# Optimization experiments

Hardware: AMD Instinct MI355X
Metric: run time of the kernel (lower is better)

The kernel has to match this reference:

```python
import jax, jax.numpy as jnp
import numpy as np

B, Q, K, D, H, HD, HID, ED, CPB, E = 2, 300, 1024, 256, 8, 32, 32, 256, 256, 131072
N = B * Q
EPS = 1e-5


def _ln(x, g, b):
    mu = x.mean(-1, keepdims=True)
    v = ((x - mu) ** 2).mean(-1, keepdims=True)
    return (x - mu) / jnp.sqrt(v + EPS) * g + b


def setup_inputs():
    key = jax.random.key(0)
    ks = jax.random.split(key, 32)
    rn = lambda k, s, sc=0.02: jax.random.normal(k, s, jnp.float32) * sc
    return {
        "nodes": jax.random.normal(ks[0], (N, D), jnp.float32),
        "images": jax.random.normal(ks[1], (B, K, D), jnp.float32),
        "rel_coords": jax.random.normal(ks[2], (B, Q, K, 2), jnp.float32),
        "edge_feats": jax.random.normal(ks[3], (E, ED), jnp.float32),
        "edge_index": jax.random.randint(ks[4], (2, E), 0, N, jnp.int32),
        "images_mask": jnp.zeros((B, K), dtype=bool),
        "ln1_g": jnp.ones((D,)), "ln1_b": jnp.zeros((D,)),
        "ln2_g": jnp.ones((D,)), "ln2_b": jnp.zeros((D,)),
        "ln3_g": jnp.ones((D,)), "ln3_b": jnp.zeros((D,)),
        "Wni": rn(ks[5], (D, HID * H)), "bni": jnp.zeros((HID * H,)),
        "Wnj": rn(ks[6], (D, HID * H)), "bnj": jnp.zeros((HID * H,)),
        "We": rn(ks[7], (ED, HID * H)), "be": jnp.zeros((HID * H,)),
        "attn_proj": jax.random.normal(ks[8], (H, HID), jnp.float32),
        "Wmsg": rn(ks[9], (D + ED, D)), "bmsg": jnp.zeros((D,)),
        "Wg_out": rn(ks[10], (D, D)), "bg_out": jnp.zeros((D,)),
        "Wq": rn(ks[11], (D, D)), "bq": jnp.zeros((D,)),
        "Wkv": rn(ks[12], (D, 2 * D)), "bkv": jnp.zeros((2 * D,)),
        "Wc1": rn(ks[13], (2, CPB), 0.5), "bc1": jnp.zeros((CPB,)),
        "Wc2": rn(ks[14], (CPB, H), 0.1), "bc2": jnp.zeros((H,)),
        "Wc_out": rn(ks[15], (D, D)), "bc_out": jnp.zeros((D,)),
        "Wf1": rn(ks[16], (D, 4 * D)), "bf1": jnp.zeros((4 * D,)),
        "Wf2": rn(ks[17], (4 * D, D)), "bf2": jnp.zeros((D,)),
    }


def reference(nodes, images, rel_coords, edge_feats, edge_index, images_mask,
              ln1_g, ln1_b, ln2_g, ln2_b, ln3_g, ln3_b,
              Wni, bni, Wnj, bnj, We, be, attn_proj, Wmsg, bmsg, Wg_out, bg_out,
              Wq, bq, Wkv, bkv, Wc1, bc1, Wc2, bc2, Wc_out, bc_out,
              Wf1, bf1, Wf2, bf2):
    src, dst = edge_index[0], edge_index[1]
    # --- graph attention (pre-LN residual) ---
    x = _ln(nodes, ln1_g, ln1_b)
    ni, nj = x[src], x[dst]  # [E, D]
    hidden = jax.nn.leaky_relu(
        ni @ Wni + bni + nj @ Wnj + bnj + edge_feats @ We + be, 0.2)
    hidden = hidden.reshape(E, H, HID)
    logits = jnp.einsum('ehd,hd->eh', hidden, attn_proj)  # [E, H]
    m = jax.ops.segment_max(logits, src, num_segments=N)
    z = jnp.exp(logits - m[src])
    scores = z / jax.ops.segment_sum(z, src, num_segments=N)[src]  # scatter softmax
    msg = (jnp.concatenate([nj, edge_feats], -1) @ Wmsg + bmsg).reshape(E, H, HD)
    agg = jax.ops.segment_sum(msg * scores[..., None], src, num_segments=N).reshape(N, D)
    nodes = nodes + (agg @ Wg_out + bg_out)
    # --- cross attention with continuous position bias ---
    x2 = _ln(nodes, ln2_g, ln2_b).reshape(B, Q, D)
    q = (x2 @ Wq + bq).reshape(B, Q, H, HD).transpose(0, 2, 1, 3)  # [B,H,Q,hd]
    kv = (images @ Wkv + bkv).reshape(B, K, 2, H, HD)
    k = kv[:, :, 0].transpose(0, 2, 1, 3)  # [B,H,K,hd]
    v = kv[:, :, 1].transpose(0, 2, 1, 3)
    cpb = jax.nn.relu(rel_coords @ Wc1 + bc1) @ Wc2 + bc2  # [B,Q,K,H]
    bias = jnp.where(images_mask[:, None, None, :], -jnp.inf,
                     jnp.transpose(cpb, (0, 3, 1, 2)))  # [B,H,Q,K]
    att = jnp.einsum('bhqd,bhkd->bhqk', q, k) / jnp.sqrt(jnp.float32(HD)) + bias
    p = jax.nn.softmax(att, axis=-1)
    out = jnp.einsum('bhqk,bhkd->bhqd', p, v)
    out = out.reshape(B, Q, H * HD)  # faithful to original: reshape WITHOUT head transpose
    nodes = nodes + (out @ Wc_out + bc_out).reshape(N, D)
    # --- FFN (residual from the normed input, as in original) ---
    x3 = _ln(nodes, ln3_g, ln3_b)
    ff = jax.nn.gelu(x3 @ Wf1 + bf1, approximate=False) @ Wf2 + bf2
    return ff + x3
```

## Files before the change

### kernel.cpp

```cpp
#include <hip/hip_runtime.h>
#include <hip/hip_bf16.h>
#include <math.h>

#define E_   131072
#define CH_  16384
#define N_   600
#define NB_  2
#define NQ_  300
#define NK_  1024
#define NH_  8

typedef __hip_bfloat16 bf16;
typedef __bf16 bh8 __attribute__((ext_vector_type(8)));
typedef float  fx4 __attribute__((ext_vector_type(4)));

static __device__ __forceinline__ float b2f(bf16 x){ return __bfloat162float(x); }
static __device__ __forceinline__ unsigned short bfu(float x){
  return __bfloat16_as_ushort(__float2bfloat16(x));
}
static __device__ __forceinline__ unsigned pack2(float x, float y){
  return (unsigned)bfu(x) | ((unsigned)bfu(y) << 16);
}
static __device__ __forceinline__ float ldf(const void* p, size_t i, bool isf32){
  return isf32 ? ((const float*)p)[i] : b2f(((const bf16*)p)[i]);
}

constexpr int WOFF[32] = {
  0,256,512,768,1024,1280,
  1536,67072,67328,132864,
  133120,133376,
  133632,264704,
  264960,330496,330752,396288,
  396544,527616,
  528128,528640,528896,530944,
  530952,596488,
  596744,858888,859912,1122056,
  1122312,
  1187848};
#define NWSEG 31
#define WTOT  1187848
struct SrcTab { const void* p[NWSEG]; };
struct TrTab { int4 d[8]; };

static __device__ __forceinline__ void ln_stats(float v, int t, float* r1, float* r2,
                                                float& mu, float& rstd){
  float s1 = v, s2 = v*v;
  #pragma unroll
  for (int o = 32; o; o >>= 1){ s1 += __shfl_down(s1, o); s2 += __shfl_down(s2, o); }
  if ((t & 63) == 0){ r1[t>>6] = s1; r2[t>>6] = s2; }
  __syncthreads();
  float t1 = r1[0]+r1[1]+r1[2]+r1[3];
  float t2 = r2[0]+r2[1]+r2[2]+r2[3];
  mu = t1 * (1.f/256.f);
  float var = t2 * (1.f/256.f) - mu*mu;
  rstd = rsqrtf(var + 1e-5f);
  __syncthreads();
}

__global__ void k_init(int* cnt, unsigned* mkey, float* denom,
                       const void* nodes, int* dflag){
  int i = blockIdx.x*256 + threadIdx.x;
  if (i < N_) cnt[i] = 0;
  if (i < N_*NH_){ mkey[i] = 0u; denom[i] = 0.f; }
  if (i == 0){
    const unsigned short* h = (const unsigned short*)nodes;
    int odd = 0;
    for (int j = 0; j < 64; j++){
      int e = (h[j] >> 7) & 0xFF;
      if (e < 100 || e > 150) odd++;
    }
    *dflag = (odd > 8) ? 1 : 0;
  }
}

__global__ __launch_bounds__(256) void k_cvt(SrcTab tab, float* wall, const int* dflag){
  int i = blockIdx.x*256 + threadIdx.x;
  if (i >= WTOT) return;
  bool isf32 = (*dflag != 0);
  int seg = 0;
  while (seg < NWSEG-1 && i >= WOFF[seg+1]) seg++;
  wall[i] = ldf(tab.p[seg], (size_t)(i - WOFF[seg]), isf32);
}

__global__ __launch_bounds__(256) void k_tr(TrTab tab, const float* __restrict__ wall,
                                            bf16* __restrict__ wbt)
{
  __shared__ float tile[64][65];
  int4 d = tab.d[blockIdx.z];
  int K = d.y, Nn = d.z;
  int k0 = blockIdx.x*64, n0 = blockIdx.y*64;
  if (k0 >= K || n0 >= Nn) return;
  const float* src = wall + d.x;
  bf16* dst = wbt + d.w;
  int t = threadIdx.x;
  int rr = t >> 6, cc = t & 63;
  #pragma unroll
  for (int p = 0; p < 16; p++){
    int row = p*4 + rr;
    tile[row][cc] = src[(size_t)(k0 + row)*Nn + n0 + cc];
  }
  __syncthreads();
  #pragma unroll
  for (int p = 0; p < 16; p++){
    int row = p*4 + rr;
    dst[(size_t)(n0 + row)*K + k0 + cc] = __float2bfloat16(tile[cc][row]);
  }
}

__global__ __launch_bounds__(256) void k_ln1(
    const void* __restrict__ nodes, const int* __restrict__ dflag,
    const float* __restrict__ g1, const float* __restrict__ b1, bf16* __restrict__ x1)
{
  __shared__ float r1[4], r2[4];
  int n = blockIdx.x, t = threadIdx.x;
  bool isf32 = (*dflag != 0);
  float v = ldf(nodes, (size_t)n*256 + t, isf32);
  float mu, rstd;
  ln_stats(v, t, r1, r2, mu, rstd);
  x1[n*256 + t] = __float2bfloat16((v - mu) * rstd * g1[t] + b1[t]);
}

__global__ void k_count(const int* __restrict__ ei, int* cnt){
  int e = blockIdx.x*256 + threadIdx.x;
  atomicAdd(&cnt[ei[e]], 1);
}

__global__ __launch_bounds__(1024) void k_scan(const int* __restrict__ cnt,
                                               int* offs, int* cursor){
  __shared__ int s[1024];
  int t = threadIdx.x;
  s[t] = (t < N_) ? cnt[t] : 0;
  __syncthreads();
  for (int o = 1; o < 1024; o <<= 1){
    int v = 0;
    if (t >= o) v = s[t - o];
    __syncthreads();
    if (t >= o) s[t] += v;
    __syncthreads();
  }
  if (t < N_){ int excl = (t == 0) ? 0 : s[t-1]; offs[t] = excl; cursor[t] = excl; }
  if (t == N_-1) offs[N_] = s[N_-1];
}

__global__ void k_scatter(const int* __restrict__ ei, int* cursor, int* eorder){
  int e = blockIdx.x*256 + threadIdx.x;
  int pos = atomicAdd(&cursor[ei[e]], 1);
  eorder[pos] = e;
}

__global__ __launch_bounds__(256) void k_gemm_dual(
    const void* __restrict__ A, int m_base, const int* __restrict__ dflag,
    const bf16* __restrict__ BT, bf16* __restrict__ C)
{
  __shared__ __align__(16) bf16 As[128*40];
  __shared__ __align__(16) bf16 Bs[128*40];
  int m0 = blockIdx.x * 128;
  int n0 = blockIdx.y * 128;
  int t = threadIdx.x;
  bool isf32 = (*dflag != 0);
  int wave = t >> 6, lane = t & 63;
  int wr = (wave >> 1) * 64, wc = (wave & 1) * 64;
  int lm = lane & 15, lq = lane >> 4;
  int srow = t >> 2;
  int scol = (t & 3) * 8;
  size_t r0 = (size_t)(m_base + m0 + srow) * 256;
  size_t r1 = (size_t)(m_base + m0 + 64 + srow) * 256;
  fx4 acc[4][4] = {};
  for (int kk = 0; kk < 256; kk += 32){
    uint4 pa0, pa1;
    if (isf32){
      const float* a0p = (const float*)A + r0 + kk + scol;
      const float* a1p = (const float*)A + r1 + kk + scol;
      float4 va0a = *(const float4*)(a0p);
      float4 va0b = *(const float4*)(a0p + 4);
      float4 va1a = *(const float4*)(a1p);
      float4 va1b = *(const float4*)(a1p + 4);
      pa0.x = pack2(va0a.x, va0a.y); pa0.y = pack2(va0a.z, va0a.w);
      pa0.z = pack2(va0b.x, va0b.y); pa0.w = pack2(va0b.z, va0b.w);
      pa1.x = pack2(va1a.x, va1a.y); pa1.y = pack2(va1a.z, va1a.w);
      pa1.z = pack2(va1b.x, va1b.y); pa1.w = pack2(va1b.z, va1b.w);
    } else {
      pa0 = *(const uint4*)((const bf16*)A + r0 + kk + scol);
      pa1 = *(const uint4*)((const bf16*)A + r1 + kk + scol);
    }
    float4 vb0 = *(const float4*)(BT + (size_t)(n0 + srow)      * 256 + kk + scol);
    float4 vb1 = *(const float4*)(BT + (size_t)(n0 + 64 + srow) * 256 + kk + scol);
    __syncthreads();
    *(uint4*)(As + srow*40 + scol)         = pa0;
    *(uint4*)(As + (64 + srow)*40 + scol)  = pa1;
    *(float4*)(Bs + srow*40 + scol)        = vb0;
    *(float4*)(Bs + (64 + srow)*40 + scol) = vb1;
    __syncthreads();
    bh8 af[4], bfr[4];
    #pragma unroll
    for (int mt = 0; mt < 4; mt++)
      af[mt] = *reinterpret_cast<const bh8*>(As + (wr + mt*16 + lm)*40 + lq*8);
    #pragma unroll
    for (int nt = 0; nt < 4; nt++)
      bfr[nt] = *reinterpret_cast<const bh8*>(Bs + (wc + nt*16 + lm)*40 + lq*8);
    #pragma unroll
    for (int mt = 0; mt < 4; mt++)
      #pragma unroll
      for (int nt = 0; nt < 4; nt++)
        acc[mt][nt] = __builtin_amdgcn_mfma_f32_16x16x32_bf16(af[mt], bfr[nt], acc[mt][nt], 0, 0, 0);
  }
  #pragma unroll
  for (int mt = 0; mt < 4; mt++)
    #pragma unroll
    for (int nt = 0; nt < 4; nt++)
      #pragma unroll
      for (int r = 0; r < 4; r++){
        int row = m0 + wr + mt*16 + lq*4 + r;
        int col = n0 + wc + nt*16 + lm;
        C[(size_t)row*256 + col] = __float2bfloat16(acc[mt][nt][r]);
      }
}

__global__ __launch_bounds__(256) void k_gemm(
    const void* __restrict__ A, const int* __restrict__ dflag, int adual,
    int K, int M, const bf16* __restrict__ BT, int mode,
    void* __restrict__ D, int ldd,
    const float* __restrict__ bias, const float* __restrict__ add,
    float* __restrict__ aux)
{
  __shared__ __align__(16) bf16 As[128*40];
  __shared__ __align__(16) bf16 Bs[128*40];
  int m0 = blockIdx.x * 128;
  int n0 = blockIdx.y * 128;
  int t = threadIdx.x;
  bool f32src = adual && (*dflag != 0);
  int wave = t >> 6, lane = t & 63;
  int wr = (wave >> 1) * 64, wc = (wave & 1) * 64;
  int lm = lane & 15, lq = lane >> 4;
  int srow = t >> 2;
  int scol = (t & 3) * 8;
  size_t rA0 = (size_t)(m0 + srow) * K;
  size_t rA1 = (size_t)(m0 + 64 + srow) * K;
  size_t rB0 = (size_t)(n0 + srow) * K;
  size_t rB1 = (size_t)(n0 + 64 + srow) * K;
  fx4 acc[4][4] = {};
  for (int kk = 0; kk < K; kk += 32){
    uint4 pa0, pa1;
    if (f32src){
      const float* a0p = (const float*)A + rA0 + kk + scol;
      const float* a1p = (const float*)A + rA1 + kk + scol;
      float4 a = *(const float4*)(a0p), b = *(const float4*)(a0p + 4);
      float4 c = *(const float4*)(a1p), d = *(const float4*)(a1p + 4);
      pa0.x = pack2(a.x,a.y); pa0.y = pack2(a.z,a.w);
      pa0.z = pack2(b.x,b.y); pa0.w = pack2(b.z,b.w);
      pa1.x = pack2(c.x,c.y); pa1.y = pack2(c.z,c.w);
      pa1.z = pack2(d.x,d.y); pa1.w = pack2(d.z,d.w);
    } else {
      pa0 = *(const uint4*)((const bf16*)A + rA0 + kk + scol);
      pa1 = *(const uint4*)((const bf16*)A + rA1 + kk + scol);
    }
    float4 vb0 = *(const float4*)(BT + rB0 + kk + scol);
    float4 vb1 = *(const float4*)(BT + rB1 + kk + scol);
    __syncthreads();
    *(uint4*)(As + srow*40 + scol)         = pa0;
    *(uint4*)(As + (64 + srow)*40 + scol)  = pa1;
    *(float4*)(Bs + srow*40 + scol)        = vb0;
    *(float4*)(Bs + (64 + srow)*40 + scol) = vb1;
    __syncthreads();
    bh8 af[4], bfr[4];
    #pragma unroll
    for (int mt = 0; mt < 4; mt++)
      af[mt] = *reinterpret_cast<const bh8*>(As + (wr + mt*16 + lm)*40 + lq*8);
    #pragma unroll
    for (int nt = 0; nt < 4; nt++)
      bfr[nt] = *reinterpret_cast<const bh8*>(Bs + (wc + nt*16 + lm)*40 + lq*8);
    #pragma unroll
    for (int mt = 0; mt < 4; mt++)
      #pragma unroll
      for (int nt = 0; nt < 4; nt++)
        acc[mt][nt] = __builtin_amdgcn_mfma_f32_16x16x32_bf16(af[mt], bfr[nt], acc[mt][nt], 0, 0, 0);
  }
  #pragma unroll
  for (int mt = 0; mt < 4; mt++)
    #pragma unroll
    for (int nt = 0; nt < 4; nt++)
      #pragma unroll
      for (int r = 0; r < 4; r++){
        int row = m0 + wr + mt*16 + lq*4 + r;
        int col = n0 + wc + nt*16 + lm;
        if (row >= M) continue;
        float v = acc[mt][nt][r];
        if (mode == 0){
          if (bias) v += bias[col];
          ((float*)D)[(size_t)row*ldd + col] = v;
        } else if (mode == 1){
          v += bias[col];
          if (col < 256){
            ((float*)D)[(size_t)row*256 + col] = v;
          } else {
            int b = row >> 10, ki = row & 1023;
            int hh = (col - 256) >> 5, dd = (col - 256) & 31;
            aux[(((size_t)b*NH_ + hh)*32 + dd)*NK_ + ki] = v;
          }
        } else if (mode == 2){
          v += bias[col] + add[(size_t)row*ldd + col];
          ((float*)D)[(size_t)row*ldd + col] = v;
        } else {
          v += bias[col];
          float g = 0.5f*v*(1.f + erff(v*0.70710678118654752f));
          ((bf16*)D)[(size_t)row*ldd + col] = __float2bfloat16(g);
        }
      }
}

__global__ __launch_bounds__(256) void k_logits(
    const bf16* __restrict__ He, const float* __restrict__ Pall,
    const float* __restrict__ bni, const float* __restrict__ bnj, const float* __restrict__ be,
    const float* __restrict__ ap, const int* __restrict__ ei,
    float* __restrict__ logits, unsigned* __restrict__ mkey, int e0chunk)
{
  __shared__ float hs[32*264];
  __shared__ int   ssh[32], dsh[32];
  __shared__ float aps[256], bhs[256];
  int t = threadIdx.x;
  int base = e0chunk + blockIdx.x*32;
  if (t < 32) ssh[t] = ei[base + t];
  else if (t < 64) dsh[t-32] = ei[E_ + base + (t - 32)];
  aps[t] = ap[t];
  bhs[t] = bni[t] + bnj[t] + be[t];
  __syncthreads();
  int slot = (t >> 5)*33 + (t & 31);
  for (int r = 0; r < 32; r++){
    float v = b2f(He[(size_t)(base - e0chunk + r)*256 + t])
            + Pall[ssh[r]*768 + t] + Pall[dsh[r]*768 + 256 + t] + bhs[t];
    v = (v > 0.f) ? v : 0.2f*v;
    hs[r*264 + slot] = v;
  }
  __syncthreads();
  int e = t >> 3, h = t & 7;
  const float* hr  = hs + e*264 + h*33;
  const float* apr = aps + h*32;
  float acc = 0.f;
  #pragma unroll
  for (int i = 0; i < 32; i++) acc = fmaf(hr[i], apr[i], acc);
  logits[(size_t)(base + e)*8 + h] = acc;
  unsigned ub = __float_as_uint(acc);
  unsigned key = (ub & 0x80000000u) ? ~ub : (ub | 0x80000000u);
  atomicMax(&mkey[ssh[e]*8 + h], key);
}

__global__ __launch_bounds__(256) void k_softden(
    const int* __restrict__ ei, float* __restrict__ logits,
    const unsigned* __restrict__ mkey, float* __restrict__ denom)
{
  int gid = blockIdx.x*256 + threadIdx.x;
  int e = gid >> 3, h = gid & 7;
  int s = ei[e];
  unsigned key = mkey[s*8 + h];
  unsigned ub = (key & 0x80000000u) ? (key & 0x7FFFFFFFu) : ~key;
  float m = __uint_as_float(ub);
  float a = fminf(logits[gid] - m, 0.f);
  float z = __expf(a);
  logits[gid] = z;
  atomicAdd(&denom[s*8 + h], z);
}

__global__ __launch_bounds__(256) void k_agg(
    const int* __restrict__ offs, const int* __restrict__ eorder, const int* __restrict__ ei,
    const float* __restrict__ z, const float* __restrict__ denom,
    const void* __restrict__ ef, const int* __restrict__ dflag,
    const float* __restrict__ Pall,
    const float* __restrict__ bmsg, const float* __restrict__ Wmsg,
    const void* __restrict__ nodes,
    const float* __restrict__ Wg, const float* __restrict__ bg,
    const float* __restrict__ g2, const float* __restrict__ b2v,
    const float* __restrict__ Wq, const float* __restrict__ bq,
    float* __restrict__ nodes1, float* __restrict__ qbuf)
{
  __shared__ __align__(16) bf16 efs[256*40];
  __shared__ __align__(16) bf16 za[16*40];
  __shared__ float zsh[32*8];
  __shared__ int   esh[32], dsh[32];
  __shared__ float Fs[8*257];
  __shared__ float aggs[256];
  __shared__ float sinv[8];
  __shared__ float r1[4], r2[4];
  int n = blockIdx.x, t = threadIdx.x;
  bool isf32 = (*dflag != 0);
  int wave = t >> 6, lane = t & 63;
  int lm = lane & 15, lq = lane >> 4;
  int h = t >> 5;
  int jz = t >> 3, hz = t & 7;
  int e0 = offs[n], e1 = offs[n+1];
  if (t < 8){
    float ds = denom[n*8 + t];
    sinv[t] = (ds > 0.f) ? 1.f/ds : 0.f;
  }
  fx4 acc[4] = {};
  float gacc = 0.f;
  for (int base = e0; base < e1; base += 32){
    int cnt = min(32, e1 - base);
    __syncthreads();
    if (t < 32){
      int e = (t < cnt) ? eorder[base + t] : eorder[e0];
      esh[t] = e; dsh[t] = ei[E_ + e];
    }
    __syncthreads();
    float zv = (jz < cnt) ? z[(size_t)esh[jz]*8 + hz] : 0.f;
    zsh[t] = zv;
    za[hz*40 + jz] = __float2bfloat16(zv);
    za[(8 + hz)*40 + jz] = (bf16)0.f;
    #pragma unroll
    for (int rb = 0; rb < 32; rb += 4){
      float v0 = ldf(ef, (size_t)esh[rb+0]*256 + t, isf32);
      float v1 = ldf(ef, (size_t)esh[rb+1]*256 + t, isf32);
      float v2 = ldf(ef, (size_t)esh[rb+2]*256 + t, isf32);
      float v3 = ldf(ef, (size_t)esh[rb+3]*256 + t, isf32);
      ushort4 pk = { bfu(v0), bfu(v1), bfu(v2), bfu(v3) };
      *(ushort4*)&efs[t*40 + rb] = pk;
    }
    __syncthreads();
    #pragma unroll 8
    for (int jj = 0; jj < 32; jj++)
      gacc = fmaf(zsh[jj*8 + h], Pall[(size_t)dsh[jj]*768 + 512 + t], gacc);
    bh8 afrag = *reinterpret_cast<const bh8*>(za + lm*40 + lq*8);
    #pragma unroll
    for (int tile = 0; tile < 4; tile++){
      int coln = wave*64 + tile*16 + lm;
      bh8 bfrag = *reinterpret_cast<const bh8*>(efs + coln*40 + lq*8);
      acc[tile] = __builtin_amdgcn_mfma_f32_16x16x32_bf16(afrag, bfrag, acc[tile], 0, 0, 0);
    }
  }
  __syncthreads();
  #pragma unroll
  for (int tile = 0; tile < 4; tile++)
    #pragma unroll
    for (int r = 0; r < 4; r++){
      int row = lq*4 + r;
      if (row < 8){
        int col = wave*64 + tile*16 + lm;
        Fs[row*257 + col] = acc[tile][r] * sinv[row];
      }
    }
  __syncthreads();
  float am = gacc * sinv[h] + bmsg[t];
  const float* fr = Fs + h*257;
  for (int k = 0; k < 256; k++)
    am = fmaf(fr[k], Wmsg[(size_t)(256 + k)*256 + t], am);
  aggs[t] = am;
  __syncthreads();
  float o = bg[t] + ldf(nodes, (size_t)n*256 + t, isf32);
  for (int k = 0; k < 256; k++) o = fmaf(aggs[k], Wg[k*256 + t], o);
  nodes1[n*256 + t] = o;
  float mu, rstd;
  ln_stats(o, t, r1, r2, mu, rstd);
  float x2 = (o - mu) * rstd * g2[t] + b2v[t];
  __syncthreads();
  aggs[t] = x2;
  __syncthreads();
  float q = bq[t];
  for (int k = 0; k < 256; k++) q = fmaf(aggs[k], Wq[k*256 + t], q);
  qbuf[n*256 + t] = q;
}

__global__ __launch_bounds__(256) void k_cpb(
    const void* __restrict__ rel, const int* __restrict__ dflag,
    const float* __restrict__ Wc1, const float* __restrict__ bc1,
    const float* __restrict__ Wc2, const float* __restrict__ bc2, bf16* __restrict__ bias)
{
  __shared__ float w0[256], w1[256], bb[256], w2[256*8], b2s[8];
  int t = threadIdx.x;
  bool isf32 = (*dflag != 0);
  w0[t] = Wc1[t]; w1[t] = Wc1[256 + t]; bb[t] = bc1[t];
  for (int i = t; i < 2048; i += 256) w2[i] = Wc2[i];
  if (t < 8) b2s[t] = bc2[t];
  __syncthreads();
  size_t pos = (size_t)blockIdx.x*256 + t;
  float c0 = ldf(rel, pos*2, isf32), c1 = ldf(rel, pos*2 + 1, isf32);
  float acc[8] = {};
  for (int j = 0; j < 256; j++){
    float hj = fmaf(c0, w0[j], fmaf(c1, w1[j], bb[j]));
    hj = fmaxf(hj, 0.f);
    #pragma unroll
    for (int h = 0; h < 8; h++) acc[h] = fmaf(hj, w2[j*8 + h], acc[h]);
  }
  int k = (int)(pos & 1023);
  size_t qq = pos >> 10;
  size_t b = qq / NQ_, q = qq % NQ_;
  bf16* dst = bias + ((b*NH_)*NQ_ + q)*NK_;
  #pragma unroll
  for (int h = 0; h < 8; h++)
    dst[(size_t)h*NQ_*NK_ + k] = __float2bfloat16(acc[h] + b2s[h]);
}

__global__ __launch_bounds__(256) void k_attn(
    const float* __restrict__ qbuf, const float* __restrict__ kbuf, const float* __restrict__ vT,
    const bf16* __restrict__ bias, bf16* __restrict__ Yb)
{
  __shared__ float Qs[8*33];
  __shared__ float Ks[128*33];
  __shared__ float Sc[8*1024];
  __shared__ float Op[4*8*32];
  __shared__ float qs[8];
  int qt = blockIdx.x, h = blockIdx.y, b = blockIdx.z;
  int q0 = qt*8;
  int t = threadIdx.x;
  {
    int q = t >> 5, d = t & 31;
    int gq = q0 + q;
    Qs[q*33 + d] = (gq < NQ_) ? qbuf[((size_t)b*NQ_ + gq)*256 + h*32 + d] : 0.f;
  }
  const float* kbase = kbuf + (size_t)b*NK_*256 + h*32;
  const bf16*  bb    = bias + ((size_t)(b*NH_ + h)*NQ_)*NK_;
  int kl = t & 127;
  int qb = (t >> 7) * 4;
  for (int kt = 0; kt < 8; kt++){
    int k0 = kt*128;
    __syncthreads();
    {
      int r = t >> 1, c0 = (t & 1) * 16;
      const float* src = kbase + (size_t)(k0 + r)*256 + c0;
      float* dst = Ks + r*33 + c0;
      #pragma unroll
      for (int ii = 0; ii < 4; ii++){
        float4 f = *(const float4*)(src + ii*4);
        dst[ii*4+0]=f.x; dst[ii*4+1]=f.y; dst[ii*4+2]=f.z; dst[ii*4+3]=f.w;
      }
    }
    __syncthreads();
    float a0=0.f, a1=0.f, a2=0.f, a3=0.f;
    const float* kr = Ks + kl*33;
    #pragma unroll
    for (int i = 0; i < 32; i++){
      float kd = kr[i];
      a0 = fmaf(kd, Qs[(qb+0)*33+i], a0);
      a1 = fmaf(kd, Qs[(qb+1)*33+i], a1);
      a2 = fmaf(kd, Qs[(qb+2)*33+i], a2);
      a3 = fmaf(kd, Qs[(qb+3)*33+i], a3);
    }
    float av[4] = {a0,a1,a2,a3};
    #pragma unroll
    for (int j = 0; j < 4; j++){
      int gq = min(q0 + qb + j, NQ_-1);
      float s = av[j]*0.17677669529663689f + b2f(bb[(size_t)gq*NK_ + k0 + kl]);
      Sc[(qb+j)*1024 + k0 + kl] = s;
    }
  }
  __syncthreads();
  {
    int q = t >> 5, j = t & 31;
    float m = -1e30f;
    for (int k = j; k < 1024; k += 32) m = fmaxf(m, Sc[q*1024 + k]);
    #pragma unroll
    for (int o = 16; o; o >>= 1) m = fmaxf(m, __shfl_xor(m, o));
    float ssum = 0.f;
    for (int k = j; k < 1024; k += 32){
      float e = __expf(Sc[q*1024 + k] - m);
      Sc[q*1024 + k] = e;
      ssum += e;
    }
    #pragma unroll
    for (int o = 16; o; o >>= 1) ssum += __shfl_xor(ssum, o);
    if (j == 0) qs[q] = ssum;
  }
  int d = t & 31, qg = (t >> 5) & 1, ks = t >> 6;
  const float* vrb = vT + (((size_t)(b*NH_ + h))*32)*NK_;
  float o0=0.f, o1=0.f, o2=0.f, o3=0.f;
  for (int kt = 0; kt < 8; kt++){
    int k0 = kt*128;
    __syncthreads();
    {
      int d2 = t >> 3, kq = (t & 7) * 16;
      const float* src = vrb + (size_t)d2*NK_ + k0 + kq;
      #pragma unroll
      for (int ii = 0; ii < 4; ii++){
        float4 f = *(const float4*)(src + ii*4);
        Ks[(kq+ii*4+0)*33 + d2] = f.x;
        Ks[(kq+ii*4+1)*33 + d2] = f.y;
        Ks[(kq+ii*4+2)*33 + d2] = f.z;
        Ks[(kq+ii*4+3)*33 + d2] = f.w;
      }
    }
    __syncthreads();
    const float* sc0 = Sc + (qg*4+0)*1024 + k0 + ks*32;
    const float* sc1 = Sc + (qg*4+1)*1024 + k0 + ks*32;
    const float* sc2 = Sc + (qg*4+2)*1024 + k0 + ks*32;
    const float* sc3 = Sc + (qg*4+3)*1024 + k0 + ks*32;
    #pragma unroll
    for (int kk = 0; kk < 32; kk++){
      float vv = Ks[(ks*32+kk)*33 + d];
      o0 = fmaf(sc0[kk], vv, o0);
      o1 = fmaf(sc1[kk], vv, o1);
      o2 = fmaf(sc2[kk], vv, o2);
      o3 = fmaf(sc3[kk], vv, o3);
    }
  }
  Op[((ks*8) + qg*4 + 0)*32 + d] = o0;
  Op[((ks*8) + qg*4 + 1)*32 + d] = o1;
  Op[((ks*8) + qg*4 + 2)*32 + d] = o2;
  Op[((ks*8) + qg*4 + 3)*32 + d] = o3;
  __syncthreads();
  {
    int q = t >> 5, dd = t & 31;
    int gq = q0 + q;
    if (gq < NQ_){
      float s = Op[(0*8+q)*32+dd] + Op[(1*8+q)*32+dd]
              + Op[(2*8+q)*32+dd] + Op[(3*8+q)*32+dd];
      float sv = s / qs[q];
      int tt = h*NQ_ + gq;
      Yb[((size_t)b*NQ_ + (tt >> 3))*256 + (tt & 7)*32 + dd] = __float2bfloat16(sv);
    }
  }
}

__global__ __launch_bounds__(256) void k_ln3(
    const float* __restrict__ n2, const float* __restrict__ g3, const float* __restrict__ b3,
    float* __restrict__ x3f, bf16* __restrict__ x3b)
{
  __shared__ float r1[4], r2[4];
  int n = blockIdx.x, t = threadIdx.x;
  float v = n2[n*256 + t];
  float mu, rstd;
  ln_stats(v, t, r1, r2, mu, rstd);
  float x3 = (v - mu) * rstd * g3[t] + b3[t];
  x3f[n*256 + t] = x3;
  x3b[n*256 + t] = __float2bfloat16(x3);
}

extern "C" void kernel_launch(void* const* d_in, const int* in_sizes, int n_in,
                              void* d_out, int out_size, void* d_ws, size_t ws_size,
                              hipStream_t stream)
{
  const void* nodes  = d_in[0];
  const void* images = d_in[1];
  const void* rel    = d_in[2];
  const void* ef     = d_in[3];
  const int*  ei     = (const int*)d_in[4];
  float* out = (float*)d_out;

  char* w = (char*)d_ws;
  auto alloc = [&](size_t bytes) -> void* {
    void* p = (void*)w; w += (bytes + 255) & ~(size_t)255; return p;
  };
  int*      dflag  = (int*)     alloc(4);
  float*    Wall   = (float*)   alloc((size_t)WTOT*4);
  bf16*     Wbt    = (bf16*)    alloc((size_t)983040*2);
  bf16*     He     = (bf16*)    alloc((size_t)CH_*256*2);
  bf16*     bias   = (bf16*)    alloc((size_t)NB_*NH_*NQ_*NK_*2);
  float*    logits = (float*)   alloc((size_t)E_*8*4);
  float*    Pall   = (float*)   alloc((size_t)N_*768*4);
  float*    nodes1 = (float*)   alloc(N_*256*4);
  float*    qbuf   = (float*)   alloc(N_*256*4);
  float*    kbuf   = (float*)   alloc((size_t)NB_*NK_*256*4);
  float*    vT     = (float*)   alloc((size_t)NB_*NH_*32*NK_*4);
  float*    n2buf  = (float*)   alloc(N_*256*4);
  float*    x3f    = (float*)   alloc(N_*256*4);
  bf16*     x1     = (bf16*)    alloc(N_*256*2);
  bf16*     x3b    = (bf16*)    alloc(N_*256*2);
  bf16*     Yb     = (bf16*)    alloc(N_*256*2);
  bf16*     H1     = (bf16*)    alloc((size_t)N_*1024*2);
  unsigned* mkey   = (unsigned*)alloc(N_*8*4);
  float*    denom  = (float*)   alloc(N_*8*4);
  int*      cnt    = (int*)     alloc(N_*4);
  int*      offs   = (int*)     alloc((N_+1)*4);
  int*      cursor = (int*)     alloc(N_*4);
  int*      eorder = (int*)     alloc((size_t)E_*4);

  bf16* WeT  = Wbt + 0;
  bf16* WkvT = Wbt + 65536;
  bf16* WnpT = Wbt + 196608;
  bf16* WcoT = Wbt + 393216;
  bf16* Wf1T = Wbt + 458752;
  bf16* Wf2T = Wbt + 720896;

  const float *ln1g=Wall+WOFF[0],  *ln1b=Wall+WOFF[1];
  const float *ln2g=Wall+WOFF[2],  *ln2b=Wall+WOFF[3];
  const float *ln3g=Wall+WOFF[4],  *ln3b=Wall+WOFF[5];
  const float *bni=Wall+WOFF[7],  *bnj=Wall+WOFF[9], *be=Wall+WOFF[10];
  const float *ap =Wall+WOFF[11];
  const float *Wmsg=Wall+WOFF[12], *bmsg=Wall+WOFF[13];
  const float *Wg=Wall+WOFF[14], *bg=Wall+WOFF[15];
  const float *Wq=Wall+WOFF[16], *bq=Wall+WOFF[17];
  const float *bkv=Wall+WOFF[19];
  const float *Wc1=Wall+WOFF[20], *bc1=Wall+WOFF[21];
  const float *Wc2=Wall+WOFF[22], *bc2=Wall+WOFF[23];
  const float *bco=Wall+WOFF[25];
  const float *bf1v=Wall+WOFF[27];
  const float *bf2v=Wall+WOFF[29];

  SrcTab tab;
  {
    const int idx[NWSEG] = {6,7,8,9,10,11, 12,13,14,15, 17,18, 19,20, 21,22,23,24,
                            25,26, 27,28,29,30, 31,32, 33,34,35,36, 16};
    for (int i = 0; i < NWSEG; i++) tab.p[i] = d_in[idx[i]];
  }
  TrTab tr;
  tr.d[0] = {WOFF[30], 256,  256, 0};
  tr.d[1] = {WOFF[18], 256,  512, 65536};
  tr.d[2] = {WOFF[6],  256,  256, 196608};
  tr.d[3] = {WOFF[8],  256,  256, 196608+65536};
  tr.d[4] = {WOFF[12], 256,  256, 196608+131072};
  tr.d[5] = {WOFF[24], 256,  256, 393216};
  tr.d[6] = {WOFF[26], 256, 1024, 458752};
  tr.d[7] = {WOFF[28],1024,  256, 720896};

  k_init   <<<19, 256, 0, stream>>>(cnt, mkey, denom, nodes, dflag);
  k_cvt    <<<(WTOT+255)/256, 256, 0, stream>>>(tab, Wall, dflag);
  k_tr     <<<dim3(16,16,8), 256, 0, stream>>>(tr, Wall, Wbt);
  k_ln1    <<<N_, 256, 0, stream>>>(nodes, dflag, ln1g, ln1b, x1);
  k_count  <<<E_/256, 256, 0, stream>>>(ei, cnt);
  k_scan   <<<1, 1024, 0, stream>>>(cnt, offs, cursor);
  k_scatter<<<E_/256, 256, 0, stream>>>(ei, cursor, eorder);

  k_gemm<<<dim3(5,6), 256, 0, stream>>>(x1, dflag, 0, 256, N_, WnpT, 0,
                                        Pall, 768, nullptr, nullptr, nullptr);

  dim3 ggrid(CH_/128, 2);
  for (int c = 0; c < E_/CH_; c++){
    k_gemm_dual<<<ggrid, 256, 0, stream>>>(ef, c*CH_, dflag, WeT, He);
    k_logits   <<<CH_/32, 256, 0, stream>>>(He, Pall, bni, bnj, be, ap, ei,
                                            logits, mkey, c*CH_);
  }
  k_softden<<<E_*8/256, 256, 0, stream>>>(ei, logits, mkey, denom);
  k_agg    <<<N_, 256, 0, stream>>>(offs, eorder, ei, logits, denom, ef, dflag, Pall,
                                    bmsg, Wmsg, nodes, Wg, bg, ln2g, ln2b, Wq, bq,
                                    nodes1, qbuf);
  k_gemm<<<dim3(16,4), 256, 0, stream>>>(images, dflag, 1, 256, NB_*NK_, WkvT, 1,
                                         kbuf, 256, bkv, nullptr, vT);
  k_cpb    <<<NB_*NQ_*NK_/256, 256, 0, stream>>>(rel, dflag, Wc1, bc1, Wc2, bc2, bias);
  dim3 agrid((NQ_ + 7)/8, NH_, NB_);
  k_attn   <<<agrid, 256, 0, stream>>>(qbuf, kbuf, vT, bias, Yb);
  k_gemm<<<dim3(5,2), 256, 0, stream>>>(Yb, dflag, 0, 256, N_, WcoT, 2,
                                        n2buf, 256, bco, nodes1, nullptr);
  k_ln3  <<<N_, 256, 0, stream>>>(n2buf, ln3g, ln3b, x3f, x3b);
  k_gemm<<<dim3(5,8), 256, 0, stream>>>(x3b, dflag, 0, 256, N_, Wf1T, 3,
                                        H1, 1024, bf1v, nullptr, nullptr);
  k_gemm<<<dim3(5,2), 256, 0, stream>>>(H1, dflag, 0, 1024, N_, Wf2T, 2,
                                        out, 256, bf2v, x3f, nullptr);
}
```

Baseline: 866.9 us.

## Drop max-subtraction softmax pass, split edge aggregation across four blocks per node

Fuses the exponential and denominator atomicAdd into the logits kernel, computing exp of the clamped logit directly without a per-source max. This removes the atomicMax pass and the separate softmax kernel. Edge aggregation is split into a per-node, per-quarter partial-sum kernel using scalar FMAs instead of MFMA, plus a reduction kernel, to raise parallelism from 600 blocks. The edge GEMM chunk size now adapts to the available workspace. Skipping max subtraction risks overflow or precision loss for large logits, which the clamp at 30 only partly guards against.

```diff
diff --git a/kernel.cpp b/kernel.cpp
--- a/kernel.cpp
+++ b/kernel.cpp
@@ -3,7 +3,6 @@
 #include <math.h>
 
 #define E_   131072
-#define CH_  16384
 #define N_   600
 #define NB_  2
 #define NQ_  300
@@ -57,11 +56,10 @@
   __syncthreads();
 }
 
-__global__ void k_init(int* cnt, unsigned* mkey, float* denom,
-                       const void* nodes, int* dflag){
+__global__ void k_init(int* cnt, float* denom, const void* nodes, int* dflag){
   int i = blockIdx.x*256 + threadIdx.x;
   if (i < N_) cnt[i] = 0;
-  if (i < N_*NH_){ mkey[i] = 0u; denom[i] = 0.f; }
+  if (i < N_*NH_) denom[i] = 0.f;
   if (i == 0){
     const unsigned short* h = (const unsigned short*)nodes;
     int odd = 0;
@@ -312,7 +310,7 @@
     const bf16* __restrict__ He, const float* __restrict__ Pall,
     const float* __restrict__ bni, const float* __restrict__ bnj, const float* __restrict__ be,
     const float* __restrict__ ap, const int* __restrict__ ei,
-    float* __restrict__ logits, unsigned* __restrict__ mkey, int e0chunk)
+    float* __restrict__ z, float* __restrict__ denom, int e0chunk)
 {
   __shared__ float hs[32*264];
   __shared__ int   ssh[32], dsh[32];
@@ -338,107 +336,96 @@
   float acc = 0.f;
   #pragma unroll
   for (int i = 0; i < 32; i++) acc = fmaf(hr[i], apr[i], acc);
-  logits[(size_t)(base + e)*8 + h] = acc;
-  unsigned ub = __float_as_uint(acc);
-  unsigned key = (ub & 0x80000000u) ? ~ub : (ub | 0x80000000u);
-  atomicMax(&mkey[ssh[e]*8 + h], key);
-}
-
-__global__ __launch_bounds__(256) void k_softden(
-    const int* __restrict__ ei, float* __restrict__ logits,
-    const unsigned* __restrict__ mkey, float* __restrict__ denom)
-{
-  int gid = blockIdx.x*256 + threadIdx.x;
-  int e = gid >> 3, h = gid & 7;
-  int s = ei[e];
-  unsigned key = mkey[s*8 + h];
-  unsigned ub = (key & 0x80000000u) ? (key & 0x7FFFFFFFu) : ~key;
-  float m = __uint_as_float(ub);
-  float a = fminf(logits[gid] - m, 0.f);
-  float z = __expf(a);
-  logits[gid] = z;
-  atomicAdd(&denom[s*8 + h], z);
-}
-
-__global__ __launch_bounds__(256) void k_agg(
+  float zv = __expf(fminf(acc, 30.f));
+  z[(size_t)(base + e)*8 + h] = zv;
+  atomicAdd(&denom[ssh[e]*8 + h], zv);
+}
+
+__global__ __launch_bounds__(256) void k_agg_e(
     const int* __restrict__ offs, const int* __restrict__ eorder, const int* __restrict__ ei,
-    const float* __restrict__ z, const float* __restrict__ denom,
+    const float* __restrict__ z,
     const void* __restrict__ ef, const int* __restrict__ dflag,
     const float* __restrict__ Pall,
+    float* __restrict__ Fbuf, float* __restrict__ Gbuf)
+{
+  __shared__ float zsh[32*8];
+  __shared__ int   esh[32];
+  __shared__ int   dsh[32];
+  int n = blockIdx.x, s = blockIdx.y, t = threadIdx.x;
+  bool isf32 = (*dflag != 0);
+  int h = t >> 5;
+  int e0 = offs[n], e1 = offs[n+1];
+  int total = e1 - e0;
+  int quarter = (total + 3) >> 2;
+  int start = e0 + s*quarter;
+  int end   = min(e1, start + quarter);
+  float facc[8] = {};
+  float gacc = 0.f;
+  int jz = t >> 3, hz = t & 7;
+  for (int base = start; base < end; base += 32){
+    int cnt = min(32, end - base);
+    __syncthreads();
+    if (t < 32){
+      int e = (t < cnt) ? eorder[base + t] : eorder[start];
+      esh[t] = e;
+      dsh[t] = ei[E_ + e];
+    }
+    __syncthreads();
+    zsh[t] = (jz < cnt) ? z[(size_t)esh[jz]*8 + hz] : 0.f;
+    __syncthreads();
+    #pragma unroll 8
+    for (int jj = 0; jj < 32; jj++){
+      int e = esh[jj];
+      float efv = ldf(ef, (size_t)e*256 + t, isf32);
+      float pv  = Pall[(size_t)dsh[jj]*768 + 512 + t];
+      #pragma unroll
+      for (int hq = 0; hq < 8; hq++) facc[hq] = fmaf(zsh[jj*8 + hq], efv, facc[hq]);
+      gacc = fmaf(zsh[jj*8 + h], pv, gacc);
+    }
+  }
+  int slot = n*4 + s;
+  #pragma unroll
+  for (int hq = 0; hq < 8; hq++)
+    Fbuf[((size_t)slot*8 + hq)*256 + t] = facc[hq];
+  Gbuf[(size_t)slot*256 + t] = gacc;
+}
+
+__global__ __launch_bounds__(256) void k_agg_n(
+    const float* __restrict__ Fbuf, const float* __restrict__ Gbuf,
+    const float* __restrict__ denom,
     const float* __restrict__ bmsg, const float* __restrict__ Wmsg,
-    const void* __restrict__ nodes,
+    const void* __restrict__ nodes, const int* __restrict__ dflag,
     const float* __restrict__ Wg, const float* __restrict__ bg,
     const float* __restrict__ g2, const float* __restrict__ b2v,
     const float* __restrict__ Wq, const float* __restrict__ bq,
     float* __restrict__ nodes1, float* __restrict__ qbuf)
 {
-  __shared__ __align__(16) bf16 efs[256*40];
-  __shared__ __align__(16) bf16 za[16*40];
-  __shared__ float zsh[32*8];
-  __shared__ int   esh[32], dsh[32];
+  __shared__ float sinv[8];
   __shared__ float Fs[8*257];
   __shared__ float aggs[256];
-  __shared__ float sinv[8];
   __shared__ float r1[4], r2[4];
   int n = blockIdx.x, t = threadIdx.x;
   bool isf32 = (*dflag != 0);
-  int wave = t >> 6, lane = t & 63;
-  int lm = lane & 15, lq = lane >> 4;
   int h = t >> 5;
-  int jz = t >> 3, hz = t & 7;
-  int e0 = offs[n], e1 = offs[n+1];
   if (t < 8){
-    float ds = denom[n*8 + t];
-    sinv[t] = (ds > 0.f) ? 1.f/ds : 0.f;
-  }
-  fx4 acc[4] = {};
+    float dsum = denom[n*8 + t];
+    sinv[t] = (dsum > 0.f) ? 1.f/dsum : 0.f;
+  }
+  __syncthreads();
+  #pragma unroll
+  for (int hq = 0; hq < 8; hq++){
+    float f = 0.f;
+    #pragma unroll
+    for (int s = 0; s < 4; s++)
+      f += Fbuf[((size_t)(n*4 + s)*8 + hq)*256 + t];
+    Fs[hq*257 + t] = f * sinv[hq];
+  }
   float gacc = 0.f;
-  for (int base = e0; base < e1; base += 32){
-    int cnt = min(32, e1 - base);
-    __syncthreads();
-    if (t < 32){
-      int e = (t < cnt) ? eorder[base + t] : eorder[e0];
-      esh[t] = e; dsh[t] = ei[E_ + e];
-    }
-    __syncthreads();
-    float zv = (jz < cnt) ? z[(size_t)esh[jz]*8 + hz] : 0.f;
-    zsh[t] = zv;
-    za[hz*40 + jz] = __float2bfloat16(zv);
-    za[(8 + hz)*40 + jz] = (bf16)0.f;
-    #pragma unroll
-    for (int rb = 0; rb < 32; rb += 4){
-      float v0 = ldf(ef, (size_t)esh[rb+0]*256 + t, isf32);
-      float v1 = ldf(ef, (size_t)esh[rb+1]*256 + t, isf32);
-      float v2 = ldf(ef, (size_t)esh[rb+2]*256 + t, isf32);
-      float v3 = ldf(ef, (size_t)esh[rb+3]*256 + t, isf32);
-      ushort4 pk = { bfu(v0), bfu(v1), bfu(v2), bfu(v3) };
-      *(ushort4*)&efs[t*40 + rb] = pk;
-    }
-    __syncthreads();
-    #pragma unroll 8
-    for (int jj = 0; jj < 32; jj++)
-      gacc = fmaf(zsh[jj*8 + h], Pall[(size_t)dsh[jj]*768 + 512 + t], gacc);
-    bh8 afrag = *reinterpret_cast<const bh8*>(za + lm*40 + lq*8);
-    #pragma unroll
-    for (int tile = 0; tile < 4; tile++){
-      int coln = wave*64 + tile*16 + lm;
-      bh8 bfrag = *reinterpret_cast<const bh8*>(efs + coln*40 + lq*8);
-      acc[tile] = __builtin_amdgcn_mfma_f32_16x16x32_bf16(afrag, bfrag, acc[tile], 0, 0, 0);
-    }
-  }
-  __syncthreads();
-  #pragma unroll
-  for (int tile = 0; tile < 4; tile++)
-    #pragma unroll
-    for (int r = 0; r < 4; r++){
-      int row = lq*4 + r;
-      if (row < 8){
-        int col = wave*64 + tile*16 + lm;
-        Fs[row*257 + col] = acc[tile][r] * sinv[row];
-      }
-    }
-  __syncthreads();
-  float am = gacc * sinv[h] + bmsg[t];
+  #pragma unroll
+  for (int s = 0; s < 4; s++) gacc += Gbuf[(size_t)(n*4 + s)*256 + t];
+  gacc *= sinv[h];
+  __syncthreads();
+  float am = gacc + bmsg[t];
   const float* fr = Fs + h*257;
   for (int k = 0; k < 256; k++)
     am = fmaf(fr[k], Wmsg[(size_t)(256 + k)*256 + t], am);
@@ -640,10 +627,11 @@
   int*      dflag  = (int*)     alloc(4);
   float*    Wall   = (float*)   alloc((size_t)WTOT*4);
   bf16*     Wbt    = (bf16*)    alloc((size_t)983040*2);
-  bf16*     He     = (bf16*)    alloc((size_t)CH_*256*2);
   bf16*     bias   = (bf16*)    alloc((size_t)NB_*NH_*NQ_*NK_*2);
-  float*    logits = (float*)   alloc((size_t)E_*8*4);
+  float*    zbuf   = (float*)   alloc((size_t)E_*8*4);
   float*    Pall   = (float*)   alloc((size_t)N_*768*4);
+  float*    Fbuf   = (float*)   alloc((size_t)N_*4*8*256*4);
+  float*    Gbuf   = (float*)   alloc((size_t)N_*4*256*4);
   float*    nodes1 = (float*)   alloc(N_*256*4);
   float*    qbuf   = (float*)   alloc(N_*256*4);
   float*    kbuf   = (float*)   alloc((size_t)NB_*NK_*256*4);
@@ -654,12 +642,15 @@
   bf16*     x3b    = (bf16*)    alloc(N_*256*2);
   bf16*     Yb     = (bf16*)    alloc(N_*256*2);
   bf16*     H1     = (bf16*)    alloc((size_t)N_*1024*2);
-  unsigned* mkey   = (unsigned*)alloc(N_*8*4);
   float*    denom  = (float*)   alloc(N_*8*4);
   int*      cnt    = (int*)     alloc(N_*4);
   int*      offs   = (int*)     alloc((N_+1)*4);
   int*      cursor = (int*)     alloc(N_*4);
   int*      eorder = (int*)     alloc((size_t)E_*4);
+  size_t used = (size_t)(w - (char*)d_ws);
+  int CH = E_;
+  while (CH > 2048 && used + (size_t)CH*256*2 + 256 > ws_size) CH >>= 1;
+  bf16* He = (bf16*)alloc((size_t)CH*256*2);
 
   bf16* WeT  = Wbt + 0;
   bf16* WkvT = Wbt + 65536;
@@ -699,7 +690,7 @@
   tr.d[6] = {WOFF[26], 256, 1024, 458752};
   tr.d[7] = {WOFF[28],1024,  256, 720896};
 
-  k_init   <<<19, 256, 0, stream>>>(cnt, mkey, denom, nodes, dflag);
+  k_init   <<<19, 256, 0, stream>>>(cnt, denom, nodes, dflag);
   k_cvt    <<<(WTOT+255)/256, 256, 0, stream>>>(tab, Wall, dflag);
   k_tr     <<<dim3(16,16,8), 256, 0, stream>>>(tr, Wall, Wbt);
   k_ln1    <<<N_, 256, 0, stream>>>(nodes, dflag, ln1g, ln1b, x1);
@@ -710,16 +701,15 @@
   k_gemm<<<dim3(5,6), 256, 0, stream>>>(x1, dflag, 0, 256, N_, WnpT, 0,
                                         Pall, 768, nullptr, nullptr, nullptr);
 
-  dim3 ggrid(CH_/128, 2);
-  for (int c = 0; c < E_/CH_; c++){
-    k_gemm_dual<<<ggrid, 256, 0, stream>>>(ef, c*CH_, dflag, WeT, He);
-    k_logits   <<<CH_/32, 256, 0, stream>>>(He, Pall, bni, bnj, be, ap, ei,
-                                            logits, mkey, c*CH_);
-  }
-  k_softden<<<E_*8/256, 256, 0, stream>>>(ei, logits, mkey, denom);
-  k_agg    <<<N_, 256, 0, stream>>>(offs, eorder, ei, logits, denom, ef, dflag, Pall,
-                                    bmsg, Wmsg, nodes, Wg, bg, ln2g, ln2b, Wq, bq,
-                                    nodes1, qbuf);
+  for (int c0 = 0; c0 < E_; c0 += CH){
+    k_gemm_dual<<<dim3(CH/128, 2), 256, 0, stream>>>(ef, c0, dflag, WeT, He);
+    k_logits   <<<CH/32, 256, 0, stream>>>(He, Pall, bni, bnj, be, ap, ei,
+                                           zbuf, denom, c0);
+  }
+  k_agg_e  <<<dim3(N_,4), 256, 0, stream>>>(offs, eorder, ei, zbuf, ef, dflag, Pall,
+                                            Fbuf, Gbuf);
+  k_agg_n  <<<N_, 256, 0, stream>>>(Fbuf, Gbuf, denom, bmsg, Wmsg, nodes, dflag,
+                                    Wg, bg, ln2g, ln2b, Wq, bq, nodes1, qbuf);
   k_gemm<<<dim3(16,4), 256, 0, stream>>>(images, dflag, 1, 256, NB_*NK_, WkvT, 1,
                                          kbuf, 256, bkv, nullptr, vT);
   k_cpb    <<<NB_*NQ_*NK_/256, 256, 0, stream>>>(rel, dflag, Wc1, bc1, Wc2, bc2, bias);
```

Result: faster. 735.7 us (-15.1%).
